# Performance work log

Hardware: AMD Instinct MI355X
Metric: run time of the kernel (lower is better)

The kernel has to match this reference:

```python
import jax, jax.numpy as jnp
import numpy as np

VOXEL_SCALE = 20.0   # cfg.SPARSE3D.VOXEL_SCALE (metric -> voxel pixels)
POOLER_SCALE = 0.25  # cfg.MODEL.ROI_BOX_HEAD.POOLER_SCALES_SPATIAL[0]
RES = 7              # pooler resolution per axis
EPS = 1e-5           # BatchNorm eps


def _roi_align_3d(feat, boxes_px, batch_idx, res):
    """3D ROIAlign, sampling_ratio=1 (one trilinear sample per bin).
    feat: [B, X, Y, Z, C] channels-last; boxes_px: [N,6] = (x1,y1,z1,x2,y2,z2)
    in feature-map coordinates. Returns [N, C, res, res, res]."""
    B, X, Y, Z, C = feat.shape
    N = boxes_px.shape[0]
    start, end = boxes_px[:, :3], boxes_px[:, 3:]
    size = jnp.maximum(end - start, 1.0)            # [N,3] legacy min roi size
    binsz = size / res
    off = jnp.arange(res, dtype=boxes_px.dtype) + 0.5
    px = start[:, 0:1] + off[None, :] * binsz[:, 0:1]   # [N,res]
    py = start[:, 1:2] + off[None, :] * binsz[:, 1:2]
    pz = start[:, 2:3] + off[None, :] * binsz[:, 2:3]
    P = res * res * res
    PX = jnp.broadcast_to(px[:, :, None, None], (N, res, res, res)).reshape(N, P)
    PY = jnp.broadcast_to(py[:, None, :, None], (N, res, res, res)).reshape(N, P)
    PZ = jnp.broadcast_to(pz[:, None, None, :], (N, res, res, res)).reshape(N, P)

    def corners(p, dim):
        p0 = jnp.floor(p)
        frac = p - p0
        i0 = jnp.clip(p0.astype(jnp.int32), 0, dim - 1)
        i1 = jnp.clip(p0.astype(jnp.int32) + 1, 0, dim - 1)
        return i0, i1, frac

    x0, x1, lx = corners(PX, X)
    y0, y1, ly = corners(PY, Y)
    z0, z1, lz = corners(PZ, Z)
    feat_flat = feat.reshape(B * X * Y * Z, C)
    base = batch_idx.astype(jnp.int32)[:, None]          # [N,1]
    acc = jnp.zeros((N, P, C), feat.dtype)
    for dx in (0, 1):  # 8 trilinear corners; fixed small loop
        xi, wx = (x0, 1.0 - lx) if dx == 0 else (x1, lx)
        for dy in (0, 1):
            yi, wy = (y0, 1.0 - ly) if dy == 0 else (y1, ly)
            for dz in (0, 1):
                zi, wz = (z0, 1.0 - lz) if dz == 0 else (z1, lz)
                lin = ((base * X + xi) * Y + yi) * Z + zi  # [N,P]
                acc = acc + (wx * wy * wz)[:, :, None] * feat_flat[lin]
    pooled = acc.reshape(N, res, res, res, C)  # 1 sample per bin -> no avg
    return pooled.transpose(0, 4, 1, 2, 3)     # [N, C, rx, ry, rz]


def setup_inputs():
    key = jax.random.key(0)
    ks = jax.random.split(key, 8)
    B, C, X, Y, Z = 2, 128, 80, 80, 20
    N, rep = 1024, 128 * RES              # rep = OUT_CHANNELS * pooler_z = 896
    in_size = C * RES * RES * RES         # 43904
    features = jax.random.normal(ks[0], (B, X, Y, Z, C), jnp.float32)
    ext = jnp.array([16.0, 16.0, 4.0], jnp.float32)  # metric extent = dim/(voxel_scale*pooler_scale)
    ctr = jax.random.uniform(ks[1], (N, 3), jnp.float32) * ext
    half = 0.25 + jax.random.uniform(ks[2], (N, 3), jnp.float32) * 1.75
    boxes = jnp.concatenate([ctr - half, ctr + half], axis=1)  # metric units
    batch_idx = jax.random.randint(ks[3], (N,), 0, B, jnp.int32)
    conv_w = jax.random.normal(ks[4], (rep, C, RES), jnp.float32) * 0.02
    conv_b = jnp.zeros((rep,), jnp.float32)
    gamma = jnp.ones((rep,), jnp.float32)
    beta = jnp.zeros((rep,), jnp.float32)
    fc6_w = jax.random.normal(ks[5], (in_size, rep), jnp.float32) * np.float32(1.0 / np.sqrt(in_size))
    fc6_b = jnp.zeros((rep,), jnp.float32)
    fc7_w = jax.random.normal(ks[6], (rep, rep), jnp.float32) * np.float32(1.0 / np.sqrt(rep))
    fc7_b = jnp.zeros((rep,), jnp.float32)
    return dict(features=features, boxes=boxes, conv_w=conv_w, conv_b=conv_b,
                gamma=gamma, beta=beta, fc6_w=fc6_w, fc6_b=fc6_b,
                fc7_w=fc7_w, fc7_b=fc7_b, batch_idx=batch_idx)


def reference(features, boxes, conv_w, conv_b, gamma, beta,
              fc6_w, fc6_b, fc7_w, fc7_b, batch_idx):
    # convert_metric_to_pixel (x voxel_scale) fused with pooler spatial scale
    boxes_px = boxes * (VOXEL_SCALE * POOLER_SCALE)
    pooled = _roi_align_3d(features, boxes_px, batch_idx, RES)  # [N,C,7,7,7]
    # conv3d kernel [1,1,Z]: contract channels and z -> [N, rep, 7, 7]
    y = jnp.einsum('ncxyz,rcz->nrxy', pooled, conv_w) + conv_b[None, :, None, None]
    # BatchNorm3d, training-mode batch statistics per channel
    mu = y.mean(axis=(0, 2, 3), keepdims=True)
    var = ((y - mu) ** 2).mean(axis=(0, 2, 3), keepdims=True)
    y = (y - mu) * jax.lax.rsqrt(var + EPS) * gamma[None, :, None, None] + beta[None, :, None, None]
    y = jax.nn.relu(y)
    x2 = y.reshape(y.shape[0], -1)                   # [N, rep*49] == [N, C*343]
    x3 = jax.nn.relu(x2 @ fc6_w + fc6_b)
    x4 = jax.nn.relu(x3 @ fc7_w + fc7_b)
    return x4
```

## Files before the change

kernel.cpp:

```cpp
#include <hip/hip_runtime.h>
#include <cstdint>

typedef unsigned short u16;
using bf16x8  = __attribute__((ext_vector_type(8))) __bf16;
using floatx4 = __attribute__((ext_vector_type(4))) float;

__device__ __forceinline__ u16 f2bf(float f) {
    uint32_t u = __builtin_bit_cast(uint32_t, f);
    u += 0x7fffu + ((u >> 16) & 1u);
    return (u16)(u >> 16);
}
__device__ __forceinline__ float bf2f(u16 h) {
    uint32_t u = ((uint32_t)h) << 16;
    return __builtin_bit_cast(float, u);
}

__device__ __forceinline__ void gload16(const u16* g, u16* l) {
    __builtin_amdgcn_global_load_lds(
        (const __attribute__((address_space(1))) unsigned int*)g,
        (__attribute__((address_space(3))) unsigned int*)l,
        16, 0, 0);
}

__global__ __launch_bounds__(256) void k_roialign(
    const float* __restrict__ feat, const float* __restrict__ boxes,
    const int* __restrict__ bidx, u16* __restrict__ A1)
{
    const int n = blockIdx.x;
    const int t = threadIdx.x;
    const float s = 5.0f;
    const float x1 = boxes[n*6+0]*s, y1 = boxes[n*6+1]*s, z1 = boxes[n*6+2]*s;
    const float x2 = boxes[n*6+3]*s, y2 = boxes[n*6+4]*s, z2 = boxes[n*6+5]*s;
    const float binx = fmaxf(x2-x1, 1.0f) * (1.0f/7.0f);
    const float biny = fmaxf(y2-y1, 1.0f) * (1.0f/7.0f);
    const float binz = fmaxf(z2-z1, 1.0f) * (1.0f/7.0f);
    const int b = bidx[n];
    const float* fb = feat + (size_t)b * 80 * 80 * 20 * 128;
    const int c4   = (t & 31) * 4;
    const int slot = t >> 5;

    for (int p = slot; p < 343; p += 8) {
        const int xq = p / 49;
        const int rem = p - xq * 49;
        const int yq = rem / 7;
        const int zq = rem - yq * 7;
        const float px = x1 + ((float)xq + 0.5f) * binx;
        const float py = y1 + ((float)yq + 0.5f) * biny;
        const float pz = z1 + ((float)zq + 0.5f) * binz;
        const float fx = floorf(px), fy = floorf(py), fz = floorf(pz);
        const float lx = px - fx, ly = py - fy, lz = pz - fz;
        const int xi0 = min(max((int)fx,     0), 79);
        const int xi1 = min(max((int)fx + 1, 0), 79);
        const int yi0 = min(max((int)fy,     0), 79);
        const int yi1 = min(max((int)fy + 1, 0), 79);
        const int zi0 = min(max((int)fz,     0), 19);
        const int zi1 = min(max((int)fz + 1, 0), 19);
        const float wx0 = 1.f-lx, wy0 = 1.f-ly, wz0 = 1.f-lz;
        const float w00 = wx0*wy0, w01 = wx0*ly, w10 = lx*wy0, w11 = lx*ly;
        float a0=0.f, a1=0.f, a2=0.f, a3=0.f;
#define RC(W, XI, YI, ZI) { \
        const float4 v = *(const float4*)(fb + (size_t)(((XI)*80+(YI))*20+(ZI))*128 + c4); \
        a0 = fmaf((W), v.x, a0); a1 = fmaf((W), v.y, a1); \
        a2 = fmaf((W), v.z, a2); a3 = fmaf((W), v.w, a3); }
        RC(w00*wz0, xi0, yi0, zi0); RC(w00*lz, xi0, yi0, zi1);
        RC(w01*wz0, xi0, yi1, zi0); RC(w01*lz, xi0, yi1, zi1);
        RC(w10*wz0, xi1, yi0, zi0); RC(w10*lz, xi1, yi0, zi1);
        RC(w11*wz0, xi1, yi1, zi0); RC(w11*lz, xi1, yi1, zi1);
#undef RC
        const int m = n * 49 + xq * 7 + yq;
        ushort4 o;
        o.x = f2bf(a0); o.y = f2bf(a1); o.z = f2bf(a2); o.w = f2bf(a3);
        *(ushort4*)(A1 + (size_t)m * 896 + zq * 128 + c4) = o;
    }
}

__global__ __launch_bounds__(256) void k_prep_wc(
    const float* __restrict__ w, u16* __restrict__ out)
{
    const int i = blockIdx.x * 256 + threadIdx.x;
    const int r = i / 896, k = i % 896;
    const int z = k >> 7, c = k & 127;
    out[i] = f2bf(w[(r * 128 + c) * 7 + z]);
}

template <int PERM>
__global__ __launch_bounds__(256) void k_transpose(
    const float* __restrict__ in, u16* __restrict__ out, int Kin)
{
    __shared__ u16 tile[64][72];
    const int kp0 = blockIdx.x * 64, r0 = blockIdx.y * 64;
    const int t = threadIdx.x;
#pragma unroll
    for (int it = 0; it < 16; ++it) {
        const int idx = it * 256 + t;
        const int i = idx >> 6, rl = idx & 63;
        const int kp = kp0 + i;
        const int k = PERM ? (kp % 896) * 49 + (kp / 896) : kp;
        tile[i][rl] = f2bf(in[(size_t)k * 896 + r0 + rl]);
    }
    __syncthreads();
#pragma unroll
    for (int it = 0; it < 16; ++it) {
        const int idx = it * 256 + t;
        const int rl = idx >> 6, i = idx & 63;
        out[(size_t)(r0 + rl) * Kin + kp0 + i] = tile[i][rl];
    }
}

template <int EPI, int SWZ>
__global__ __launch_bounds__(256) void k_gemm(
    const u16* __restrict__ A, const u16* __restrict__ Bt,
    float* __restrict__ outF, u16* __restrict__ outH,
    const float* __restrict__ bias, float* __restrict__ bnsum, float* __restrict__ bnsq,
    int Astride, int Bstride, int kpc, int ktot, int partStride)
{
    __shared__ __align__(16) u16 lA[3 * 4096];
    __shared__ __align__(16) u16 lB[3 * 4096];
    const int t = threadIdx.x;
    const int wave = t >> 6, lane = t & 63;
    const int wm = wave & 1, wn = wave >> 1;
    const int quad = lane >> 4, lr = lane & 15;

    int mt, nt, kz;
    if (SWZ == 1) {
        const int wg = blockIdx.x;
        const int swz = (wg & 7) * 343 + (wg >> 3);
        nt = swz % 7; mt = swz / 7; kz = 0;
    } else if (SWZ == 2) {
        const int wg = blockIdx.x;
        const int xcd = wg & 7, local = wg >> 3;
        const int kzl = local / 56, rem = local % 56;
        kz = xcd * 3 + kzl;
        nt = rem >> 3; mt = rem & 7;
    } else {
        mt = blockIdx.x; nt = blockIdx.y; kz = blockIdx.z;
    }
    const size_t m0 = (size_t)mt * 128;
    const size_t n0 = (size_t)nt * 128;
    const int kbeg = kz * kpc;
    const int kend = min(kbeg + kpc, ktot);
    const int nstep = kend - kbeg;

    floatx4 acc[4][4];
    const floatx4 zero = {0.f, 0.f, 0.f, 0.f};
#pragma unroll
    for (int a = 0; a < 4; ++a)
#pragma unroll
        for (int bq = 0; bq < 4; ++bq) acc[a][bq] = zero;

    const int ch0 = wave * 2, ch1 = ch0 + 1;
    const int sr0 = ch0 * 16 + (lane >> 2);
    const int sr1 = sr0 + 16;
    const int sc  = (lane & 3) * 8;
    const u16* gA0 = A  + (m0 + sr0) * (size_t)Astride + (size_t)kbeg * 32 + sc;
    const u16* gA1 = A  + (m0 + sr1) * (size_t)Astride + (size_t)kbeg * 32 + sc;
    const u16* gB0 = Bt + (n0 + sr0) * (size_t)Bstride + (size_t)kbeg * 32 + sc;
    const u16* gB1 = Bt + (n0 + sr1) * (size_t)Bstride + (size_t)kbeg * 32 + sc;
    const int lo0 = ch0 * 512, lo1 = ch1 * 512;

#define STAGE(la_, lb_) { \
    gload16(gA0, (la_) + lo0); gload16(gA1, (la_) + lo1); \
    gload16(gB0, (lb_) + lo0); gload16(gB1, (lb_) + lo1); \
    gA0 += 32; gA1 += 32; gB0 += 32; gB1 += 32; }

    u16 *pA0 = lA, *pA1 = lA + 4096, *pA2 = lA + 8192;
    u16 *pB0 = lB, *pB1 = lB + 4096, *pB2 = lB + 8192;

    STAGE(pA0, pB0);
    if (nstep > 1) STAGE(pA1, pB1);

    for (int ts = 0; ts < nstep; ++ts) {
        if (ts + 1 < nstep) {
            asm volatile("s_waitcnt vmcnt(4)" ::: "memory");
        } else {
            asm volatile("s_waitcnt vmcnt(0)" ::: "memory");
        }
        __builtin_amdgcn_sched_barrier(0);
        __builtin_amdgcn_s_barrier();
        if (ts + 2 < nstep) STAGE(pA2, pB2);
        asm volatile("" ::: "memory");
        bf16x8 af[4], bfr[4];
#pragma unroll
        for (int mt4 = 0; mt4 < 4; ++mt4)
            af[mt4] = *(const bf16x8*)(pA0 + (wm * 64 + mt4 * 16 + lr) * 32 + quad * 8);
#pragma unroll
        for (int nt4 = 0; nt4 < 4; ++nt4)
            bfr[nt4] = *(const bf16x8*)(pB0 + (wn * 64 + nt4 * 16 + lr) * 32 + quad * 8);
#pragma unroll
        for (int mt4 = 0; mt4 < 4; ++mt4)
#pragma unroll
            for (int nt4 = 0; nt4 < 4; ++nt4)
                acc[mt4][nt4] = __builtin_amdgcn_mfma_f32_16x16x32_bf16(
                    af[mt4], bfr[nt4], acc[mt4][nt4], 0, 0, 0);
        u16* tp;
        tp = pA0; pA0 = pA1; pA1 = pA2; pA2 = tp;
        tp = pB0; pB0 = pB1; pB1 = pB2; pB2 = tp;
    }
#undef STAGE

    if (EPI == 0) {
#pragma unroll
        for (int nt4 = 0; nt4 < 4; ++nt4) {
            const int n = (int)n0 + wn * 64 + nt4 * 16 + lr;
            const float bv = bias[n];
            float s1 = 0.f, s2 = 0.f;
#pragma unroll
            for (int mt4 = 0; mt4 < 4; ++mt4) {
#pragma unroll
                for (int j = 0; j < 4; ++j) {
                    const int m = (int)m0 + wm * 64 + mt4 * 16 + quad * 4 + j;
                    const float v = acc[mt4][nt4][j] + bv;
                    outH[(size_t)m * 896 + n] = f2bf(v);
                    s1 += v;
                    s2 = fmaf(v, v, s2);
                }
            }
            s1 += __shfl_xor(s1, 16); s1 += __shfl_xor(s1, 32);
            s2 += __shfl_xor(s2, 16); s2 += __shfl_xor(s2, 32);
            if (quad == 0) {
                atomicAdd(&bnsum[n], s1);
                atomicAdd(&bnsq[n],  s2);
            }
        }
    } else {
        float* po = outF + (size_t)kz * partStride;
#pragma unroll
        for (int nt4 = 0; nt4 < 4; ++nt4) {
            const int n = (int)n0 + wn * 64 + nt4 * 16 + lr;
#pragma unroll
            for (int mt4 = 0; mt4 < 4; ++mt4) {
#pragma unroll
                for (int j = 0; j < 4; ++j) {
                    const int m = (int)m0 + wm * 64 + mt4 * 16 + quad * 4 + j;
                    po[(size_t)m * 896 + n] = acc[mt4][nt4][j];
                }
            }
        }
    }
}

__global__ __launch_bounds__(256) void k_bn_apply(
    u16* __restrict__ y, const float* __restrict__ s1, const float* __restrict__ s2,
    const float* __restrict__ gamma, const float* __restrict__ beta)
{
    const size_t i = ((size_t)blockIdx.x * 256 + threadIdx.x) * 8;
    uint4 d = *(const uint4*)(y + i);
    const u16* h = (const u16*)&d;
    const int r0 = (int)(i % 896);
    __align__(16) u16 o[8];
    const float invM = 1.0f / 50176.0f;
#pragma unroll
    for (int j = 0; j < 8; ++j) {
        const int r = r0 + j;
        const float mu  = s1[r] * invM;
        const float var = fmaf(-mu, mu, s2[r] * invM);
        const float rs  = rsqrtf(var + 1e-5f);
        const float v   = (bf2f(h[j]) - mu) * rs * gamma[r] + beta[r];
        o[j] = f2bf(fmaxf(v, 0.f));
    }
    *(uint4*)(y + i) = *(const uint4*)o;
}

__global__ __launch_bounds__(256) void k_x3(
    const float* __restrict__ part, const float* __restrict__ bias, u16* __restrict__ x3)
{
    const size_t i = ((size_t)blockIdx.x * 256 + threadIdx.x) * 4;
    float a0=0.f, a1=0.f, a2=0.f, a3=0.f;
#pragma unroll
    for (int c = 0; c < 24; ++c) {
        const float4 v = *(const float4*)(part + (size_t)c * 917504 + i);
        a0 += v.x; a1 += v.y; a2 += v.z; a3 += v.w;
    }
    const int r = (int)(i % 896);
    ushort4 o;
    o.x = f2bf(fmaxf(a0 + bias[r+0], 0.f));
    o.y = f2bf(fmaxf(a1 + bias[r+1], 0.f));
    o.z = f2bf(fmaxf(a2 + bias[r+2], 0.f));
    o.w = f2bf(fmaxf(a3 + bias[r+3], 0.f));
    *(ushort4*)(x3 + i) = o;
}

__global__ __launch_bounds__(256) void k_out(
    const float* __restrict__ part, const float* __restrict__ bias, float* __restrict__ out)
{
    const size_t i = ((size_t)blockIdx.x * 256 + threadIdx.x) * 4;
    float a0=0.f, a1=0.f, a2=0.f, a3=0.f;
#pragma unroll
    for (int c = 0; c < 7; ++c) {
        const float4 v = *(const float4*)(part + (size_t)c * 917504 + i);
        a0 += v.x; a1 += v.y; a2 += v.z; a3 += v.w;
    }
    const int r = (int)(i % 896);
    float4 o;
    o.x = fmaxf(a0 + bias[r+0], 0.f);
    o.y = fmaxf(a1 + bias[r+1], 0.f);
    o.z = fmaxf(a2 + bias[r+2], 0.f);
    o.w = fmaxf(a3 + bias[r+3], 0.f);
    *(float4*)(out + i) = o;
}

extern "C" void kernel_launch(void* const* d_in, const int* in_sizes, int n_in,
                              void* d_out, int out_size, void* d_ws, size_t ws_size,
                              hipStream_t stream)
{
    (void)in_sizes; (void)n_in; (void)out_size; (void)ws_size;
    const float* features = (const float*)d_in[0];
    const float* boxes    = (const float*)d_in[1];
    const float* conv_w   = (const float*)d_in[2];
    const float* conv_b   = (const float*)d_in[3];
    const float* gamma    = (const float*)d_in[4];
    const float* beta     = (const float*)d_in[5];
    const float* fc6_w    = (const float*)d_in[6];
    const float* fc6_b    = (const float*)d_in[7];
    const float* fc7_w    = (const float*)d_in[8];
    const float* fc7_b    = (const float*)d_in[9];
    const int*   batch_idx = (const int*)d_in[10];
    float* out = (float*)d_out;
    char* ws = (char*)d_ws;

    size_t off = 0;
    auto alloc = [&](size_t b) { size_t o = off; off += (b + 255) & ~(size_t)255; return o; };
    const size_t oA1   = alloc(50176ull * 896 * 2);
    const size_t oWcT  = alloc(896ull * 896 * 2);
    const size_t oY    = alloc(50176ull * 896 * 2);
    const size_t oF6T  = alloc(43904ull * 896 * 2);
    const size_t oF7T  = alloc(896ull * 896 * 2);
    const size_t oStat = alloc(8192);
    const size_t oP2 = oA1;
    const size_t oX3 = oA1 + 88080384;
    const size_t oP3 = oA1;

    u16*   A1    = (u16*)(ws + oA1);
    u16*   WcT   = (u16*)(ws + oWcT);
    u16*   Y     = (u16*)(ws + oY);
    u16*   F6T   = (u16*)(ws + oF6T);
    u16*   F7T   = (u16*)(ws + oF7T);
    float* bnsum = (float*)(ws + oStat);
    float* bnsq  = bnsum + 1024;
    float* P2    = (float*)(ws + oP2);
    u16*   X3    = (u16*)(ws + oX3);
    float* P3    = (float*)(ws + oP3);

    k_prep_wc<<<3136, 256, 0, stream>>>(conv_w, WcT);
    k_transpose<1><<<dim3(686, 14), 256, 0, stream>>>(fc6_w, F6T, 43904);
    k_transpose<0><<<dim3(14, 14), 256, 0, stream>>>(fc7_w, F7T, 896);
    hipMemsetAsync(ws + oStat, 0, 8192, stream);

    k_roialign<<<1024, 256, 0, stream>>>(features, boxes, batch_idx, A1);

    k_gemm<0, 1><<<dim3(2744, 1, 1), 256, 0, stream>>>(
        A1, WcT, nullptr, Y, conv_b, bnsum, bnsq, 896, 896, 28, 28, 0);

    k_bn_apply<<<21952, 256, 0, stream>>>(Y, bnsum, bnsq, gamma, beta);

    k_gemm<1, 2><<<dim3(1344, 1, 1), 256, 0, stream>>>(
        Y, F6T, P2, nullptr, nullptr, nullptr, nullptr, 43904, 43904, 58, 1372, 917504);
    k_x3<<<896, 256, 0, stream>>>(P2, fc6_b, X3);

    k_gemm<1, 0><<<dim3(8, 7, 7), 256, 0, stream>>>(
        X3, F7T, P3, nullptr, nullptr, nullptr, nullptr, 896, 896, 4, 28, 917504);
    k_out<<<896, 256, 0, stream>>>(P3, fc7_b, out);
}
```

Before: 751.5 us.

## Enlarge GEMM tiles to 256x128 with 8 waves and re-split K partitions

The GEMM kernel now uses 512 threads (8 waves) and a 256x128 output tile, so the B tile is loaded once and reused across twice as many A rows. The XCD swizzles are recomputed for the smaller grids, and the fc6 split-K drops from 24 to 18 partitions, which means fewer partial sums for k_x3 to reduce. In exchange each workgroup uses more LDS, the grids become smaller (504 blocks for fc6), and occupancy and load balance may suffer.

```diff
diff --git a/kernel.cpp b/kernel.cpp
--- a/kernel.cpp
+++ b/kernel.cpp
@@ -108,34 +108,37 @@
 }
 
 template <int EPI, int SWZ>
-__global__ __launch_bounds__(256) void k_gemm(
+__global__ __launch_bounds__(512) void k_gemm(
     const u16* __restrict__ A, const u16* __restrict__ Bt,
     float* __restrict__ outF, u16* __restrict__ outH,
     const float* __restrict__ bias, float* __restrict__ bnsum, float* __restrict__ bnsq,
     int Astride, int Bstride, int kpc, int ktot, int partStride)
 {
-    __shared__ __align__(16) u16 lA[3 * 4096];
+    __shared__ __align__(16) u16 lA[3 * 8192];
     __shared__ __align__(16) u16 lB[3 * 4096];
     const int t = threadIdx.x;
     const int wave = t >> 6, lane = t & 63;
-    const int wm = wave & 1, wn = wave >> 1;
+    const int wm = wave >> 1, wn = wave & 1;
     const int quad = lane >> 4, lr = lane & 15;
 
     int mt, nt, kz;
     if (SWZ == 1) {
         const int wg = blockIdx.x;
-        const int swz = (wg & 7) * 343 + (wg >> 3);
+        const int xcd = wg & 7, i = wg >> 3;
+        const int q = 171, r = 4;
+        const int base = (xcd < r) ? xcd * (q + 1) : r * (q + 1) + (xcd - r) * q;
+        const int swz = base + i;
         nt = swz % 7; mt = swz / 7; kz = 0;
     } else if (SWZ == 2) {
         const int wg = blockIdx.x;
-        const int xcd = wg & 7, local = wg >> 3;
-        const int kzl = local / 56, rem = local % 56;
-        kz = xcd * 3 + kzl;
-        nt = rem >> 3; mt = rem & 7;
+        const int g = (wg & 7) * 63 + (wg >> 3);
+        kz = g / 28;
+        const int rem = g % 28;
+        nt = rem >> 2; mt = rem & 3;
     } else {
         mt = blockIdx.x; nt = blockIdx.y; kz = blockIdx.z;
     }
-    const size_t m0 = (size_t)mt * 128;
+    const size_t m0 = (size_t)mt * 256;
     const size_t n0 = (size_t)nt * 128;
     const int kbeg = kz * kpc;
     const int kend = min(kbeg + kpc, ktot);
@@ -148,22 +151,22 @@
 #pragma unroll
         for (int bq = 0; bq < 4; ++bq) acc[a][bq] = zero;
 
-    const int ch0 = wave * 2, ch1 = ch0 + 1;
-    const int sr0 = ch0 * 16 + (lane >> 2);
-    const int sr1 = sr0 + 16;
-    const int sc  = (lane & 3) * 8;
-    const u16* gA0 = A  + (m0 + sr0) * (size_t)Astride + (size_t)kbeg * 32 + sc;
-    const u16* gA1 = A  + (m0 + sr1) * (size_t)Astride + (size_t)kbeg * 32 + sc;
-    const u16* gB0 = Bt + (n0 + sr0) * (size_t)Bstride + (size_t)kbeg * 32 + sc;
-    const u16* gB1 = Bt + (n0 + sr1) * (size_t)Bstride + (size_t)kbeg * 32 + sc;
-    const int lo0 = ch0 * 512, lo1 = ch1 * 512;
+    const int chA0 = wave * 2, chA1 = chA0 + 1, chB = wave;
+    const int srA0 = chA0 * 16 + (lane >> 2);
+    const int srA1 = srA0 + 16;
+    const int srB  = chB * 16 + (lane >> 2);
+    const int sc   = (lane & 3) * 8;
+    const u16* gA0 = A  + (m0 + srA0) * (size_t)Astride + (size_t)kbeg * 32 + sc;
+    const u16* gA1 = A  + (m0 + srA1) * (size_t)Astride + (size_t)kbeg * 32 + sc;
+    const u16* gB0 = Bt + (n0 + srB ) * (size_t)Bstride + (size_t)kbeg * 32 + sc;
+    const int loA0 = chA0 * 512, loA1 = chA1 * 512, loB = chB * 512;
 
 #define STAGE(la_, lb_) { \
-    gload16(gA0, (la_) + lo0); gload16(gA1, (la_) + lo1); \
-    gload16(gB0, (lb_) + lo0); gload16(gB1, (lb_) + lo1); \
-    gA0 += 32; gA1 += 32; gB0 += 32; gB1 += 32; }
-
-    u16 *pA0 = lA, *pA1 = lA + 4096, *pA2 = lA + 8192;
+    gload16(gA0, (la_) + loA0); gload16(gA1, (la_) + loA1); \
+    gload16(gB0, (lb_) + loB); \
+    gA0 += 32; gA1 += 32; gB0 += 32; }
+
+    u16 *pA0 = lA, *pA1 = lA + 8192, *pA2 = lA + 16384;
     u16 *pB0 = lB, *pB1 = lB + 4096, *pB2 = lB + 8192;
 
     STAGE(pA0, pB0);
@@ -171,7 +174,7 @@
 
     for (int ts = 0; ts < nstep; ++ts) {
         if (ts + 1 < nstep) {
-            asm volatile("s_waitcnt vmcnt(4)" ::: "memory");
+            asm volatile("s_waitcnt vmcnt(3)" ::: "memory");
         } else {
             asm volatile("s_waitcnt vmcnt(0)" ::: "memory");
         }
@@ -267,7 +270,7 @@
     const size_t i = ((size_t)blockIdx.x * 256 + threadIdx.x) * 4;
     float a0=0.f, a1=0.f, a2=0.f, a3=0.f;
 #pragma unroll
-    for (int c = 0; c < 24; ++c) {
+    for (int c = 0; c < 18; ++c) {
         const float4 v = *(const float4*)(part + (size_t)c * 917504 + i);
         a0 += v.x; a1 += v.y; a2 += v.z; a3 += v.w;
     }
@@ -327,7 +330,7 @@
     const size_t oF7T  = alloc(896ull * 896 * 2);
     const size_t oStat = alloc(8192);
     const size_t oP2 = oA1;
-    const size_t oX3 = oA1 + 88080384;
+    const size_t oX3 = oA1 + 66060288;
     const size_t oP3 = oA1;
 
     u16*   A1    = (u16*)(ws + oA1);
@@ -348,16 +351,16 @@
 
     k_roialign<<<1024, 256, 0, stream>>>(features, boxes, batch_idx, A1);
 
-    k_gemm<0, 1><<<dim3(2744, 1, 1), 256, 0, stream>>>(
+    k_gemm<0, 1><<<dim3(1372, 1, 1), 512, 0, stream>>>(
         A1, WcT, nullptr, Y, conv_b, bnsum, bnsq, 896, 896, 28, 28, 0);
 
     k_bn_apply<<<21952, 256, 0, stream>>>(Y, bnsum, bnsq, gamma, beta);
 
-    k_gemm<1, 2><<<dim3(1344, 1, 1), 256, 0, stream>>>(
-        Y, F6T, P2, nullptr, nullptr, nullptr, nullptr, 43904, 43904, 58, 1372, 917504);
+    k_gemm<1, 2><<<dim3(504, 1, 1), 512, 0, stream>>>(
+        Y, F6T, P2, nullptr, nullptr, nullptr, nullptr, 43904, 43904, 77, 1372, 917504);
     k_x3<<<896, 256, 0, stream>>>(P2, fc6_b, X3);
 
-    k_gemm<1, 0><<<dim3(8, 7, 7), 256, 0, stream>>>(
+    k_gemm<1, 0><<<dim3(4, 7, 7), 512, 0, stream>>>(
         X3, F7T, P3, nullptr, nullptr, nullptr, nullptr, 896, 896, 4, 28, 917504);
     k_out<<<896, 256, 0, stream>>>(P3, fc7_b, out);
 }
```

New measurement: 708.1 us. 5.8% less time.
